# Kernel tuning notes

Hardware: AMD Instinct MI355X
Metric: run time of the kernel (lower is better)

## Reference

```python
import jax, jax.numpy as jnp
import numpy as np

NUM_HEADS = 8
ROPE_BASE = 10000.0


def _rope(x):
    # x: [b, n, c]; RoPE with channel_dims=(n,), feature_dim=c, k_max=c//2
    b, n, c = x.shape
    k_max = c // 2
    theta = 1.0 / (ROPE_BASE ** (jnp.arange(k_max, dtype=jnp.float32) / k_max))
    angles = jnp.arange(n, dtype=jnp.float32)[:, None] * theta  # [n, k_max]
    cos = jnp.cos(angles)
    sin = jnp.sin(angles)
    xr = x[..., 0::2]  # real parts  [b, n, k_max]
    xi = x[..., 1::2]  # imag parts
    pr = cos * xr - sin * xi
    pi = cos * xi + sin * xr
    # original concatenates real half then imag half (no re-interleave)
    return jnp.concatenate([pr, pi], axis=-1)


def setup_inputs() -> dict:
    key = jax.random.key(0)
    ks = jax.random.split(key, 5)
    b, n, c = 4, 4096, 1024
    x = jax.random.normal(ks[0], (b, n, c), dtype=jnp.float32)
    qk_w = jax.random.normal(ks[1], (c, 2 * c), dtype=jnp.float32) * (1.0 / np.sqrt(c))
    qk_b = jnp.zeros((2 * c,), dtype=jnp.float32)
    lepe_w = jax.random.normal(ks[2], (3, c, c), dtype=jnp.float32) * (1.0 / np.sqrt(3 * c))  # [W, I, O]
    lepe_b = jnp.zeros((c,), dtype=jnp.float32)
    return {"x": x, "qk_w": qk_w, "qk_b": qk_b, "lepe_w": lepe_w, "lepe_b": lepe_b}


def reference(x, qk_w, qk_b, lepe_w, lepe_b):
    b, n, c = x.shape
    h = NUM_HEADS
    d = c // h

    qk = x @ qk_w + qk_b
    q, k = jnp.split(qk, 2, axis=-1)
    q = jax.nn.elu(q) + 1.0
    k = jax.nn.elu(k) + 1.0

    q_rope = _rope(q)
    k_rope = _rope(k)

    def to_heads(t):  # [b, n, c] -> [b, h, n, d]
        return t.reshape(b, n, h, d).transpose(0, 2, 1, 3)

    qh = to_heads(q)
    kh = to_heads(k)
    qr = to_heads(q_rope)
    kr = to_heads(k_rope)
    vh = to_heads(x)

    # z = 1 / (q . mean_n(k) + eps)  -> [b, h, n, 1]
    k_mean = jnp.mean(kh, axis=2, keepdims=True)  # [b, h, 1, d]
    z = 1.0 / (jnp.einsum('bhnd,bhmd->bhnm', qh, k_mean) + 1e-6)

    # kv = k_rope^T v / sqrt(n)  -> [b, h, d, d]
    kv = jnp.einsum('bhnd,bhne->bhde', kr, vh) * (1.0 / jnp.sqrt(jnp.float32(n)))
    out = jnp.einsum('bhnd,bhde->bhne', qr, kv) * z  # [b, h, n, d]

    out = out.transpose(0, 2, 1, 3).reshape(b, n, c)

    # lepe: Conv1D(dim, 3, padding='same') applied to v (== original x)
    lepe = jax.lax.conv_general_dilated(
        x, lepe_w, window_strides=(1,), padding='SAME',
        dimension_numbers=('NWC', 'WIO', 'NWC')) + lepe_b
    return out + lepe
```

## Files before the change

### kernel.cpp

```cpp
#include <hip/hip_runtime.h>
#include <cmath>

#define BB 4
#define NN 4096
#define CC 1024
#define HH 8
#define DD 128
#define MM (BB*NN)
#define NP (NN+2)

typedef __attribute__((ext_vector_type(8))) short bf16x8;
typedef __attribute__((ext_vector_type(4))) float f32x4;

static __device__ __forceinline__ unsigned short f2bf(float f) {
    unsigned int u = __float_as_uint(f);
    unsigned int r = (u + 0x7FFF + ((u >> 16) & 1)) >> 16;
    return (unsigned short)r;
}
static __device__ __forceinline__ float bf2f(short s) {
    return __uint_as_float(((unsigned int)(unsigned short)s) << 16);
}
static __device__ __forceinline__ float4 bf4(ushort4 u) {
    float4 f;
    f.x = __uint_as_float((unsigned int)u.x << 16);
    f.y = __uint_as_float((unsigned int)u.y << 16);
    f.z = __uint_as_float((unsigned int)u.z << 16);
    f.w = __uint_as_float((unsigned int)u.w << 16);
    return f;
}

static __device__ __forceinline__ void load_lds16(const void* g, void* l) {
    __builtin_amdgcn_global_load_lds(
        (const __attribute__((address_space(1))) unsigned int*)g,
        (__attribute__((address_space(3))) unsigned int*)l, 16, 0, 0);
}

static __device__ __forceinline__ int swz(int row, int ko) {
    return (row * 64 + ko) ^ ((row & 7) << 3);
}

#define CFENCE() asm volatile("" ::: "memory")
#define BAR() do { CFENCE(); __builtin_amdgcn_s_barrier(); CFENCE(); } while (0)

__global__ __launch_bounds__(256) void padx_kernel(
    const float* __restrict__ x, unsigned short* __restrict__ xpad)
{
    const int r = blockIdx.x;
    const int b = r / NP, p = r % NP;
    const int c = threadIdx.x * 4;
    ushort4 v = {0, 0, 0, 0};
    if (p >= 1 && p <= NN) {
        const float4 f = *(const float4*)&x[(size_t)(b * NN + p - 1) * CC + c];
        v.x = f2bf(f.x); v.y = f2bf(f.y); v.z = f2bf(f.z); v.w = f2bf(f.w);
    }
    *(ushort4*)&xpad[(size_t)r * CC + c] = v;
}

__global__ __launch_bounds__(256) void transpose_bf16_kernel(
    const float* __restrict__ src, unsigned short* __restrict__ dst,
    int R, int Cc)
{
    __shared__ float t[32][33];
    const int r0 = blockIdx.y * 32, c0 = blockIdx.x * 32;
    const int tx = threadIdx.x & 31, ty = threadIdx.x >> 5;
    #pragma unroll
    for (int i = 0; i < 4; ++i) {
        int r = ty + i * 8;
        t[r][tx] = src[(size_t)(r0 + r) * Cc + c0 + tx];
    }
    __syncthreads();
    #pragma unroll
    for (int i = 0; i < 4; ++i) {
        int r = ty + i * 8;
        dst[(size_t)(c0 + r) * R + r0 + tx] = f2bf(t[tx][r]);
    }
}

static __device__ __forceinline__ void stage_half(
    const unsigned short* __restrict__ g, int stride,
    unsigned short* lds, int tid)
{
    const int wb = tid & ~63;
    #pragma unroll
    for (int l = 0; l < 2; ++l) {
        const int c = l * 512 + tid;
        const int row = c >> 3;
        const int col8 = (c & 7) ^ (row & 7);
        load_lds16(&g[(size_t)row * stride + col8 * 8],
                   &lds[(size_t)(l * 512 + wb) * 8]);
    }
}

static __device__ __forceinline__ void lda4(
    const unsigned short* __restrict__ h, int lr0, int rl, int ko, bf16x8* o)
{
    #pragma unroll
    for (int i = 0; i < 4; ++i)
        o[i] = *(const bf16x8*)&h[swz(lr0 + i * 16 + rl, ko)];
}

static __device__ __forceinline__ void mfma_quad(
    f32x4 (*acc)[4], int mfb, const bf16x8* af, const bf16x8* bfr)
{
    __builtin_amdgcn_s_setprio(1);
    #pragma unroll
    for (int i = 0; i < 4; ++i)
        #pragma unroll
        for (int nf = 0; nf < 4; ++nf)
            acc[mfb + i][nf] = __builtin_amdgcn_mfma_f32_16x16x32_bf16(
                af[i], bfr[nf], acc[mfb + i][nf], 0, 0, 0);
    __builtin_amdgcn_s_setprio(0);
}

static __device__ __forceinline__ void mfma_ktile(
    const unsigned short* __restrict__ Ah, const unsigned short* __restrict__ Bh,
    int blr0, int rl, int kq, f32x4 acc[8][4])
{
    __builtin_amdgcn_s_setprio(1);
    #pragma unroll
    for (int ks = 0; ks < 2; ++ks) {
        const int ko = ks * 32 + kq;
        bf16x8 af[8], bfr[4];
        lda4(Ah, 0, rl, ko, af);
        lda4(Ah, 64, rl, ko, af + 4);
        lda4(Bh, blr0, rl, ko, bfr);
        #pragma unroll
        for (int mf = 0; mf < 8; ++mf)
            #pragma unroll
            for (int nf = 0; nf < 4; ++nf)
                acc[mf][nf] = __builtin_amdgcn_mfma_f32_16x16x32_bf16(
                    af[mf], bfr[nf], acc[mf][nf], 0, 0, 0);
    }
    __builtin_amdgcn_s_setprio(0);
}

#define KTILE_4PHASE(Ah, Bh, blr0, STAGE_A0, STAGE_A1, STAGE_B0, STAGE_B1, HAVE_NEXT) \
    do {                                                                     \
        bf16x8 af_[4], af2_[4], bfr_[4], bfr2_[4];                           \
        if (HAVE_NEXT) {                                                     \
            STAGE_A0;                                                        \
            asm volatile("s_waitcnt vmcnt(2)" ::: "memory");                 \
        } else {                                                             \
            asm volatile("s_waitcnt vmcnt(0)" ::: "memory");                 \
        }                                                                    \
        BAR();                                                               \
        lda4(Ah, 0, rl, ko0, af_);                                           \
        lda4(Bh, blr0, rl, ko0, bfr_);                                       \
        mfma_quad(acc, 0, af_, bfr_);                                        \
        BAR();                                                               \
        lda4(Ah, 64, rl, ko0, af2_);                                         \
        if (HAVE_NEXT) { STAGE_A1; }                                         \
        BAR();                                                               \
        mfma_quad(acc, 4, af2_, bfr_);                                       \
        BAR();                                                               \
        lda4(Ah, 0, rl, ko1, af_);                                           \
        lda4(Bh, blr0, rl, ko1, bfr2_);                                      \
        if (HAVE_NEXT) { STAGE_B0; }                                         \
        BAR();                                                               \
        mfma_quad(acc, 0, af_, bfr2_);                                       \
        BAR();                                                               \
        lda4(Ah, 64, rl, ko1, af2_);                                         \
        if (HAVE_NEXT) { STAGE_B1; }                                         \
        BAR();                                                               \
        mfma_quad(acc, 4, af2_, bfr2_);                                      \
        BAR();                                                               \
    } while (0)

__global__ __launch_bounds__(512) void gemm_qk_mfma(
    const unsigned short* __restrict__ xpad, const unsigned short* __restrict__ wT,
    const float* __restrict__ bias, unsigned short* __restrict__ qbuf,
    unsigned short* __restrict__ qrbuf, unsigned short* __restrict__ krP,
    float* __restrict__ ksum)
{
    __shared__ __align__(16) unsigned short SA[2][2][8192];
    __shared__ __align__(16) unsigned short SB[2][2][8192];
    const int m0 = blockIdx.x * 256;
    const int n0 = blockIdx.y * 256;
    const int tid = threadIdx.x;
    const int lane = tid & 63;
    const int wv = tid >> 6;
    const int wr = wv >> 2, wc = wv & 3;
    const int b = m0 >> 12;
    const int rbase = m0 + 1 + 2 * b;
    const int rl = lane & 15;
    const int kq = (lane >> 4) * 8;
    const int blr0 = (wc & 1) * 64;

    const unsigned short* Agl = &xpad[(size_t)rbase * CC];
    const unsigned short* Bgl = &wT[(size_t)n0 * CC];

    f32x4 acc[8][4] = {};
    stage_half(Agl, CC, SA[0][0], tid);
    stage_half(&Agl[(size_t)128 * CC], CC, SA[0][1], tid);
    stage_half(Bgl, CC, SB[0][0], tid);
    stage_half(&Bgl[(size_t)128 * CC], CC, SB[0][1], tid);

    const int NT = 16;
    for (int t = 0; t < NT; ++t) {
        const int cur = t & 1;
        if (t + 1 < NT) {
            const int k1 = (t + 1) * 64;
            stage_half(&Agl[k1], CC, SA[cur ^ 1][0], tid);
            stage_half(&Agl[(size_t)128 * CC + k1], CC, SA[cur ^ 1][1], tid);
            stage_half(&Bgl[k1], CC, SB[cur ^ 1][0], tid);
            stage_half(&Bgl[(size_t)128 * CC + k1], CC, SB[cur ^ 1][1], tid);
            asm volatile("s_waitcnt vmcnt(8)" ::: "memory");
        } else {
            asm volatile("s_waitcnt vmcnt(0)" ::: "memory");
        }
        BAR();
        mfma_ktile(SA[cur][wr], SB[cur][wc >> 1], blr0, rl, kq, acc);
        BAR();
    }

    const bool khalf = (n0 >= CC);
    const int col = lane & 15, rb4 = (lane >> 4) * 4;
    #pragma unroll
    for (int nf = 0; nf < 4; ++nf) {
        const int n = n0 + wc * 64 + nf * 16 + col;
        const float bn = bias[n];
        const int jpair = (khalf ? (n - CC) : n) >> 1;
        const float theta = __builtin_exp2f((float)jpair * (-13.287712379549449f / 512.0f));
        const bool odd = (n & 1) != 0;
        float csum = 0.0f;
        #pragma unroll
        for (int mf = 0; mf < 8; ++mf)
            #pragma unroll
            for (int r = 0; r < 4; ++r) {
                const int m = m0 + wr * 128 + mf * 16 + rb4 + r;
                float v = acc[mf][nf][r] + bn;
                v = (v > 0.0f) ? (v + 1.0f) : __expf(v);
                csum += v;
                const float p = __shfl_xor(v, 1);
                float sv, cv;
                __sincosf((float)(m & (NN - 1)) * theta, &sv, &cv);
                const float rot = odd ? (cv * v + sv * p) : (cv * v - sv * p);
                if (!khalf) {
                    qbuf[(size_t)m * CC + n] = f2bf(v);
                    const int qcol = odd ? (512 + jpair) : jpair;
                    qrbuf[(size_t)m * CC + qcol] = f2bf(rot);
                } else {
                    const int kc = n - CC;
                    const int h = kc >> 7;
                    const int jj = jpair & 63;
                    krP[((size_t)(b * 8 + (odd ? 4 : 0) + (h >> 1)) * NN + (m & (NN - 1))) * DD
                        + (h & 1) * 64 + jj] = f2bf(rot);
                }
            }
        if (khalf) atomicAdd(&ksum[b * CC + (n - CC)], csum);
    }
}

__global__ __launch_bounds__(256) void z_kernel(
    const unsigned short* __restrict__ qbuf, const float* __restrict__ ksum,
    float* __restrict__ zbuf)
{
    const int tid = threadIdx.x;
    const int row = tid >> 3;
    const int h = tid & 7;
    const int m = blockIdx.x * 32 + row;
    const int b = m >> 12;
    const unsigned short* qrow = qbuf + (size_t)m * CC + h * DD;
    const float* km = ksum + b * CC + h * DD;
    float dot = 0.0f;
    #pragma unroll
    for (int i = 0; i < 16; ++i) {
        const bf16x8 qv = *(const bf16x8*)&qrow[i * 8];
        #pragma unroll
        for (int jq = 0; jq < 8; ++jq)
            dot = fmaf(bf2f(qv[jq]), km[i * 8 + jq], dot);
    }
    dot *= (1.0f / (float)NN);
    zbuf[(size_t)m * HH + h] = 1.0f / (dot + 1e-6f);
}

__global__ __launch_bounds__(256) void kv_kernel(
    const unsigned short* __restrict__ krP, const unsigned short* __restrict__ xpad,
    float* __restrict__ kvpart)
{
    __shared__ float ksm[8][132];
    __shared__ float vsm[8][132];
    const int bh = blockIdx.x;
    const int slice = blockIdx.y;
    const int b = bh >> 3, h = bh & 7;
    const int n0 = slice * 256;
    const int tid = threadIdx.x;
    const int td = (tid >> 4) * 8;
    const int te = (tid & 15) * 8;
    const unsigned short* kp = krP + ((size_t)bh * NN + n0) * DD;
    const unsigned short* vp = xpad + ((size_t)(b * NP) + 1 + n0) * CC + h * DD;
    const int sr = tid >> 5;
    const int sc = (tid & 31) * 4;
    float acc[8][8] = {};
    ushort4 kq = *(const ushort4*)&kp[(size_t)sr * DD + sc];
    ushort4 vq = *(const ushort4*)&vp[(size_t)sr * CC + sc];
    for (int r0 = 0; r0 < 256; r0 += 8) {
        *(float4*)&ksm[sr][sc] = bf4(kq);
        *(float4*)&vsm[sr][sc] = bf4(vq);
        __syncthreads();
        if (r0 + 8 < 256) {
            kq = *(const ushort4*)&kp[(size_t)(r0 + 8 + sr) * DD + sc];
            vq = *(const ushort4*)&vp[(size_t)(r0 + 8 + sr) * CC + sc];
        }
        #pragma unroll
        for (int r = 0; r < 8; ++r) {
            float a[8], bv[8];
            *(float4*)&a[0]  = *(const float4*)&ksm[r][td];
            *(float4*)&a[4]  = *(const float4*)&ksm[r][td + 4];
            *(float4*)&bv[0] = *(const float4*)&vsm[r][te];
            *(float4*)&bv[4] = *(const float4*)&vsm[r][te + 4];
            #pragma unroll
            for (int i = 0; i < 8; ++i)
                #pragma unroll
                for (int j = 0; j < 8; ++j)
                    acc[i][j] = fmaf(a[i], bv[j], acc[i][j]);
        }
        __syncthreads();
    }
    float* op = kvpart + ((size_t)slice * 32 + bh) * (DD * DD);
    #pragma unroll
    for (int i = 0; i < 8; ++i)
        #pragma unroll
        for (int j = 0; j < 8; j += 4)
            *(float4*)&op[(td + i) * DD + te + j] = *(float4*)&acc[i][j];
}

__global__ __launch_bounds__(256) void kv_reduce_t_kernel(
    const float* __restrict__ kvpart, unsigned short* __restrict__ kvT)
{
    __shared__ float t[32][33];
    const int bh = blockIdx.y;
    const int dblk = blockIdx.x >> 2, eblk = blockIdx.x & 3;
    const int tx = threadIdx.x & 31, ty = threadIdx.x >> 5;
    #pragma unroll
    for (int i = 0; i < 4; ++i) {
        const int d = dblk * 32 + ty + i * 8;
        float s = 0.0f;
        #pragma unroll
        for (int sl = 0; sl < 16; ++sl)
            s += kvpart[((size_t)sl * 32 + bh) * (DD * DD) + (size_t)d * DD + eblk * 32 + tx];
        t[ty + i * 8][tx] = s * (1.0f / 64.0f);
    }
    __syncthreads();
    #pragma unroll
    for (int i = 0; i < 4; ++i) {
        const int e = ty + i * 8;
        kvT[((size_t)bh * DD + eblk * 32 + e) * DD + dblk * 32 + tx] = f2bf(t[tx][e]);
    }
}

__global__ __launch_bounds__(512) void lepe_mfma(
    const unsigned short* __restrict__ xpad, const unsigned short* __restrict__ wT,
    const float* __restrict__ bias, const unsigned short* __restrict__ qr,
    const unsigned short* __restrict__ kvT, const float* __restrict__ z,
    float* __restrict__ out)
{
    __shared__ __align__(16) unsigned short SA[2][2][8192];
    __shared__ __align__(16) unsigned short SB[2][2][8192];
    const int m0 = blockIdx.x * 256;
    const int n0 = blockIdx.y * 256;
    const int tid = threadIdx.x;
    const int lane = tid & 63;
    const int wv = tid >> 6;
    const int wr = wv >> 2, wc = wv & 3;
    const int b = m0 >> 12;
    const int rbase = m0 + 1 + 2 * b;
    const int rl = lane & 15;
    const int ko0 = (lane >> 4) * 8;
    const int ko1 = 32 + ko0;
    const int blr0 = (wc & 1) * 64;
    const int rb4 = (lane >> 4) * 4;
    const int h0 = n0 >> 7;
    const int hw = h0 + (wc >> 1);

    f32x4 acc[8][4] = {};

    #pragma unroll
    for (int kt = 0; kt < 2; ++kt) {
        stage_half(&qr[(size_t)m0 * CC + h0 * DD + kt * 64], CC, SA[0][0], tid);
        stage_half(&qr[(size_t)(m0 + 128) * CC + h0 * DD + kt * 64], CC, SA[0][1], tid);
        stage_half(&qr[(size_t)m0 * CC + (h0 + 1) * DD + kt * 64], CC, SA[1][0], tid);
        stage_half(&qr[(size_t)(m0 + 128) * CC + (h0 + 1) * DD + kt * 64], CC, SA[1][1], tid);
        stage_half(&kvT[(size_t)(b * 8 + h0) * DD * DD + kt * 64], DD, SB[0][0], tid);
        stage_half(&kvT[(size_t)(b * 8 + h0) * DD * DD + (size_t)128 * DD + kt * 64], DD, SB[0][1], tid);
        __syncthreads();
        mfma_ktile(SA[wc >> 1][wr], SB[0][wc >> 1], blr0, rl, ko0, acc);
        __syncthreads();
    }

    #pragma unroll
    for (int mf = 0; mf < 8; ++mf)
        #pragma unroll
        for (int r = 0; r < 4; ++r) {
            const float zz = z[(size_t)(m0 + wr * 128 + mf * 16 + rb4 + r) * HH + hw];
            #pragma unroll
            for (int nf = 0; nf < 4; ++nf)
                acc[mf][nf][r] *= zz;
        }
    asm volatile("s_waitcnt vmcnt(0)" ::: "memory");

    const unsigned short* Bgl = &wT[(size_t)n0 * (3 * CC)];
    {
        const unsigned short* A0 = &xpad[(size_t)(rbase - 1) * CC];
        stage_half(A0, CC, SA[0][0], tid);
        stage_half(&A0[(size_t)128 * CC], CC, SA[0][1], tid);
        stage_half(Bgl, 3 * CC, SB[0][0], tid);
        stage_half(&Bgl[(size_t)128 * (3 * CC)], 3 * CC, SB[0][1], tid);
    }
    const int NT = 48;
    for (int t = 0; t < NT; ++t) {
        const int cur = t & 1;
        const unsigned short* Ah = SA[cur][wr];
        const unsigned short* Bh = SB[cur][wc >> 1];
        const int k1 = (t + 1) * 64;
        const int sh1 = (k1 >> 10) - 1;
        const int i1 = k1 & (CC - 1);
        const unsigned short* An = &xpad[(size_t)(rbase + sh1) * CC + i1];
        KTILE_4PHASE(Ah, Bh, blr0,
            stage_half(An, CC, SA[cur ^ 1][0], tid),
            stage_half(&An[(size_t)128 * CC], CC, SA[cur ^ 1][1], tid),
            stage_half(&Bgl[k1], 3 * CC, SB[cur ^ 1][0], tid),
            stage_half(&Bgl[(size_t)128 * (3 * CC) + k1], 3 * CC, SB[cur ^ 1][1], tid),
            (t + 1 < NT));
    }

    const int col = lane & 15;
    #pragma unroll
    for (int nf = 0; nf < 4; ++nf) {
        const int n = n0 + wc * 64 + nf * 16 + col;
        const float bn = bias[n];
        #pragma unroll
        for (int mf = 0; mf < 8; ++mf)
            #pragma unroll
            for (int r = 0; r < 4; ++r) {
                const int m = m0 + wr * 128 + mf * 16 + rb4 + r;
                out[(size_t)m * CC + n] = acc[mf][nf][r] + bn;
            }
    }
}

extern "C" void kernel_launch(void* const* d_in, const int* in_sizes, int n_in,
                              void* d_out, int out_size, void* d_ws, size_t ws_size,
                              hipStream_t stream)
{
    const float* x      = (const float*)d_in[0];
    const float* qk_w   = (const float*)d_in[1];
    const float* qk_b   = (const float*)d_in[2];
    const float* lepe_w = (const float*)d_in[3];
    const float* lepe_b = (const float*)d_in[4];
    float* out = (float*)d_out;

    float* ws     = (float*)d_ws;
    float* zbuf   = ws;
    float* ksum   = zbuf + (size_t)MM * HH;
    float* kvpart = ksum + (size_t)BB * CC;
    unsigned short* xpad  = (unsigned short*)(kvpart + (size_t)16 * 32 * DD * DD);
    unsigned short* wqT   = xpad + (size_t)BB * NP * CC;
    unsigned short* wlT   = wqT + (size_t)2 * CC * CC;
    unsigned short* qbuf  = wlT + (size_t)CC * 3 * CC;
    unsigned short* qrbuf = qbuf + (size_t)MM * CC;
    unsigned short* krP   = qrbuf + (size_t)MM * CC;
    unsigned short* kvT   = krP + (size_t)32 * NN * DD;

    hipMemsetAsync(ksum, 0, BB * CC * sizeof(float), stream);

    padx_kernel          <<<BB * NP,                      256, 0, stream>>>(x, xpad);
    transpose_bf16_kernel<<<dim3(2 * CC / 32, CC / 32),   256, 0, stream>>>(qk_w, wqT, CC, 2 * CC);
    transpose_bf16_kernel<<<dim3(CC / 32, 3 * CC / 32),   256, 0, stream>>>(lepe_w, wlT, 3 * CC, CC);

    gemm_qk_mfma      <<<dim3(MM / 256, 2048 / 256), 512, 0, stream>>>(xpad, wqT, qk_b, qbuf, qrbuf, krP, ksum);
    z_kernel          <<<MM / 32,                    256, 0, stream>>>(qbuf, ksum, zbuf);
    kv_kernel         <<<dim3(32, 16),               256, 0, stream>>>(krP, xpad, kvpart);
    kv_reduce_t_kernel<<<dim3(16, 32),               256, 0, stream>>>(kvpart, kvT);
    lepe_mfma         <<<dim3(MM / 256, CC / 256),   512, 0, stream>>>(xpad, wlT, lepe_b, qrbuf, kvT, zbuf, out);
}
```

Baseline: 488.4 us.

## Drop unrotated q buffer; stage rotated outputs through LDS for coalesced stores

The QK GEMM epilogue no longer writes the unrotated q buffer. The z kernel instead recovers q·mean(k) from rotated q by applying the inverse rotation to the k mean (computing sin/cos per element). Rotated q/k values are written into shared memory first, then stored as 16-byte vectors, replacing the scattered 2-byte global stores. This cuts a 32MB bf16 write and read and improves store coalescing, at the cost of extra transcendental work in z_kernel and a different bf16 rounding path for z.

Result: faster. 440.2 us (-9.9%).

```diff
diff --git a/kernel.cpp b/kernel.cpp
--- a/kernel.cpp
+++ b/kernel.cpp
@@ -168,12 +168,12 @@
 
 __global__ __launch_bounds__(512) void gemm_qk_mfma(
     const unsigned short* __restrict__ xpad, const unsigned short* __restrict__ wT,
-    const float* __restrict__ bias, unsigned short* __restrict__ qbuf,
-    unsigned short* __restrict__ qrbuf, unsigned short* __restrict__ krP,
-    float* __restrict__ ksum)
-{
-    __shared__ __align__(16) unsigned short SA[2][2][8192];
-    __shared__ __align__(16) unsigned short SB[2][2][8192];
+    const float* __restrict__ bias, unsigned short* __restrict__ qrbuf,
+    unsigned short* __restrict__ krP, float* __restrict__ ksum)
+{
+    __shared__ __align__(16) unsigned short SMEM[65536];
+    #define SAP(buf, half) (&SMEM[(buf) * 16384 + (half) * 8192])
+    #define SBP(buf, half) (&SMEM[32768 + (buf) * 16384 + (half) * 8192])
     const int m0 = blockIdx.x * 256;
     const int n0 = blockIdx.y * 256;
     const int tid = threadIdx.x;
@@ -190,34 +190,39 @@
     const unsigned short* Bgl = &wT[(size_t)n0 * CC];
 
     f32x4 acc[8][4] = {};
-    stage_half(Agl, CC, SA[0][0], tid);
-    stage_half(&Agl[(size_t)128 * CC], CC, SA[0][1], tid);
-    stage_half(Bgl, CC, SB[0][0], tid);
-    stage_half(&Bgl[(size_t)128 * CC], CC, SB[0][1], tid);
+    stage_half(Agl, CC, SAP(0, 0), tid);
+    stage_half(&Agl[(size_t)128 * CC], CC, SAP(0, 1), tid);
+    stage_half(Bgl, CC, SBP(0, 0), tid);
+    stage_half(&Bgl[(size_t)128 * CC], CC, SBP(0, 1), tid);
 
     const int NT = 16;
     for (int t = 0; t < NT; ++t) {
         const int cur = t & 1;
         if (t + 1 < NT) {
             const int k1 = (t + 1) * 64;
-            stage_half(&Agl[k1], CC, SA[cur ^ 1][0], tid);
-            stage_half(&Agl[(size_t)128 * CC + k1], CC, SA[cur ^ 1][1], tid);
-            stage_half(&Bgl[k1], CC, SB[cur ^ 1][0], tid);
-            stage_half(&Bgl[(size_t)128 * CC + k1], CC, SB[cur ^ 1][1], tid);
+            stage_half(&Agl[k1], CC, SAP(cur ^ 1, 0), tid);
+            stage_half(&Agl[(size_t)128 * CC + k1], CC, SAP(cur ^ 1, 1), tid);
+            stage_half(&Bgl[k1], CC, SBP(cur ^ 1, 0), tid);
+            stage_half(&Bgl[(size_t)128 * CC + k1], CC, SBP(cur ^ 1, 1), tid);
             asm volatile("s_waitcnt vmcnt(8)" ::: "memory");
         } else {
             asm volatile("s_waitcnt vmcnt(0)" ::: "memory");
         }
         BAR();
-        mfma_ktile(SA[cur][wr], SB[cur][wc >> 1], blr0, rl, kq, acc);
+        mfma_ktile(SAP(cur, wr), SBP(cur, wc >> 1), blr0, rl, kq, acc);
         BAR();
     }
 
+    unsigned short* T = SMEM;
     const bool khalf = (n0 >= CC);
     const int col = lane & 15, rb4 = (lane >> 4) * 4;
+    const int pos0 = m0 & (NN - 1);
+    const int P = b * 8 + (khalf ? ((n0 - CC) >> 8) : 0);
+
     #pragma unroll
     for (int nf = 0; nf < 4; ++nf) {
-        const int n = n0 + wc * 64 + nf * 16 + col;
+        const int lcol = wc * 64 + nf * 16 + col;
+        const int n = n0 + lcol;
         const float bn = bias[n];
         const int jpair = (khalf ? (n - CC) : n) >> 1;
         const float theta = __builtin_exp2f((float)jpair * (-13.287712379549449f / 512.0f));
@@ -227,7 +232,8 @@
         for (int mf = 0; mf < 8; ++mf)
             #pragma unroll
             for (int r = 0; r < 4; ++r) {
-                const int m = m0 + wr * 128 + mf * 16 + rb4 + r;
+                const int lrow = wr * 128 + mf * 16 + rb4 + r;
+                const int m = m0 + lrow;
                 float v = acc[mf][nf][r] + bn;
                 v = (v > 0.0f) ? (v + 1.0f) : __expf(v);
                 csum += v;
@@ -235,24 +241,31 @@
                 float sv, cv;
                 __sincosf((float)(m & (NN - 1)) * theta, &sv, &cv);
                 const float rot = odd ? (cv * v + sv * p) : (cv * v - sv * p);
-                if (!khalf) {
-                    qbuf[(size_t)m * CC + n] = f2bf(v);
-                    const int qcol = odd ? (512 + jpair) : jpair;
-                    qrbuf[(size_t)m * CC + qcol] = f2bf(rot);
-                } else {
-                    const int kc = n - CC;
-                    const int h = kc >> 7;
-                    const int jj = jpair & 63;
-                    krP[((size_t)(b * 8 + (odd ? 4 : 0) + (h >> 1)) * NN + (m & (NN - 1))) * DD
-                        + (h & 1) * 64 + jj] = f2bf(rot);
-                }
+                T[lrow * 256 + (odd ? 128 : 0) + (lcol >> 1)] = f2bf(rot);
             }
         if (khalf) atomicAdd(&ksum[b * CC + (n - CC)], csum);
     }
+    __syncthreads();
+
+    #pragma unroll
+    for (int pss = 0; pss < 16; ++pss) {
+        const int ch = pss * 512 + tid;
+        const int row = ch >> 5;
+        const int cx = ch & 31;
+        const int stripe = cx >> 4;
+        const int c8 = (cx & 15) * 8;
+        const bf16x8 w = *(const bf16x8*)&T[row * 256 + cx * 8];
+        if (!khalf)
+            *(bf16x8*)&qrbuf[(size_t)(m0 + row) * CC + stripe * 512 + (n0 >> 1) + c8] = w;
+        else
+            *(bf16x8*)&krP[((size_t)(P + stripe * 4) * NN + pos0 + row) * DD + c8] = w;
+    }
+    #undef SAP
+    #undef SBP
 }
 
 __global__ __launch_bounds__(256) void z_kernel(
-    const unsigned short* __restrict__ qbuf, const float* __restrict__ ksum,
+    const unsigned short* __restrict__ qr, const float* __restrict__ ksum,
     float* __restrict__ zbuf)
 {
     const int tid = threadIdx.x;
@@ -260,15 +273,26 @@
     const int h = tid & 7;
     const int m = blockIdx.x * 32 + row;
     const int b = m >> 12;
-    const unsigned short* qrow = qbuf + (size_t)m * CC + h * DD;
+    const int pos = m & (NN - 1);
+    const unsigned short* qe = qr + (size_t)m * CC + h * 64;
+    const unsigned short* qo = qe + 512;
     const float* km = ksum + b * CC + h * DD;
     float dot = 0.0f;
     #pragma unroll
-    for (int i = 0; i < 16; ++i) {
-        const bf16x8 qv = *(const bf16x8*)&qrow[i * 8];
-        #pragma unroll
-        for (int jq = 0; jq < 8; ++jq)
-            dot = fmaf(bf2f(qv[jq]), km[i * 8 + jq], dot);
+    for (int j8 = 0; j8 < 8; ++j8) {
+        const bf16x8 ev = *(const bf16x8*)&qe[j8 * 8];
+        const bf16x8 ov = *(const bf16x8*)&qo[j8 * 8];
+        #pragma unroll
+        for (int u = 0; u < 8; ++u) {
+            const int jj = j8 * 8 + u;
+            const int jg = h * 64 + jj;
+            const float theta = __builtin_exp2f((float)jg * (-13.287712379549449f / 512.0f));
+            float sv, cv;
+            __sincosf((float)pos * theta, &sv, &cv);
+            const float k0 = km[2 * jj], k1 = km[2 * jj + 1];
+            dot = fmaf(bf2f(ev[u]), cv * k0 - sv * k1, dot);
+            dot = fmaf(bf2f(ov[u]), cv * k1 + sv * k0, dot);
+        }
     }
     dot *= (1.0f / (float)NN);
     zbuf[(size_t)m * HH + h] = 1.0f / (dot + 1e-6f);
@@ -457,19 +481,18 @@
     unsigned short* xpad  = (unsigned short*)(kvpart + (size_t)16 * 32 * DD * DD);
     unsigned short* wqT   = xpad + (size_t)BB * NP * CC;
     unsigned short* wlT   = wqT + (size_t)2 * CC * CC;
-    unsigned short* qbuf  = wlT + (size_t)CC * 3 * CC;
-    unsigned short* qrbuf = qbuf + (size_t)MM * CC;
+    unsigned short* qrbuf = wlT + (size_t)CC * 3 * CC;
     unsigned short* krP   = qrbuf + (size_t)MM * CC;
     unsigned short* kvT   = krP + (size_t)32 * NN * DD;
 
-    hipMemsetAsync(ksum, 0, BB * CC * sizeof(float), stream);
+    (void)hipMemsetAsync(ksum, 0, BB * CC * sizeof(float), stream);
 
     padx_kernel          <<<BB * NP,                      256, 0, stream>>>(x, xpad);
     transpose_bf16_kernel<<<dim3(2 * CC / 32, CC / 32),   256, 0, stream>>>(qk_w, wqT, CC, 2 * CC);
     transpose_bf16_kernel<<<dim3(CC / 32, 3 * CC / 32),   256, 0, stream>>>(lepe_w, wlT, 3 * CC, CC);
 
-    gemm_qk_mfma      <<<dim3(MM / 256, 2048 / 256), 512, 0, stream>>>(xpad, wqT, qk_b, qbuf, qrbuf, krP, ksum);
-    z_kernel          <<<MM / 32,                    256, 0, stream>>>(qbuf, ksum, zbuf);
+    gemm_qk_mfma      <<<dim3(MM / 256, 2048 / 256), 512, 0, stream>>>(xpad, wqT, qk_b, qrbuf, krP, ksum);
+    z_kernel          <<<MM / 32,                    256, 0, stream>>>(qrbuf, ksum, zbuf);
     kv_kernel         <<<dim3(32, 16),               256, 0, stream>>>(krP, xpad, kvpart);
     kv_reduce_t_kernel<<<dim3(16, 32),               256, 0, stream>>>(kvpart, kvT);
     lepe_mfma         <<<dim3(MM / 256, CC / 256),   512, 0, stream>>>(xpad, wlT, lepe_b, qrbuf, kvT, zbuf, out);
```
